# Kernel tuning notes

Hardware: AMD Instinct MI355X
Metric: run time of the kernel (lower is better)

The kernel has to match this reference:

```python
import jax, jax.numpy as jnp
import numpy as np

B, C, N, K, OUT = 8, 64, 40962, 7, 64

def setup_inputs() -> dict:
    key = jax.random.key(0)
    k1, k2, k3, k4 = jax.random.split(key, 4)
    x = jax.random.normal(k1, (B, C, N), dtype=jnp.float32)
    neigh_orders = jax.random.randint(k2, (K * N,), 0, N, dtype=jnp.int64)
    # nn.Linear(7*C, OUT): W [OUT, 7*C], b [OUT]
    W = jax.random.normal(k3, (OUT, K * C), dtype=jnp.float32) * (1.0 / np.sqrt(K * C))
    b = jax.random.normal(k4, (OUT,), dtype=jnp.float32) * 0.01
    return {"x": x, "neigh_orders": neigh_orders, "W": W, "b": b}

def reference(x, neigh_orders, W, b):
    Bn, Cn, Nn = x.shape
    # gather 7-ring neighborhood: [B, C, N*7] -> [B, C, N, 7]
    mat = x[:, :, neigh_orders].reshape(Bn, Cn, Nn, K)
    # torch flattens (7, C) with 7 outer after permute -> W reshaped to [OUT, 7, C]
    W3 = W.reshape(W.shape[0], K, Cn)
    # fused gather-GEMM: [B,C,N,7] x [O,7,C] -> [B,O,N]
    out = jnp.einsum('bcnk,okc->bon', mat, W3) + b[None, :, None]
    return out
```

## Files before the change

kernel.cpp:

```cpp
#include <hip/hip_runtime.h>
#include <hip/hip_bf16.h>

#define Bn   8
#define Cn   64
#define Nn   40962
#define Kn   7
#define OUTn 64
#define NVT  641

typedef __bf16 bf16x8 __attribute__((ext_vector_type(8)));
typedef __bf16 bf16x4 __attribute__((ext_vector_type(4)));
typedef float  f32x4  __attribute__((ext_vector_type(4)));

__global__ __launch_bounds__(256) void transpose_kernel(
    const float* __restrict__ x, __bf16* __restrict__ xT,
    const float* __restrict__ W, __bf16* __restrict__ Wb, int b0)
{
    __shared__ unsigned int tile[64][65];
    const int tid  = threadIdx.x;
    const int lane = tid & 63;
    const int w    = tid >> 6;
    const int n0   = blockIdx.x * 128;
    const int bl   = blockIdx.y;
    const int b    = b0 + bl;
    const size_t xb = (size_t)b * Cn * Nn;

    if (bl == 0) {
        const int wi = blockIdx.x * 256 + tid;
        if (wi < OUTn * Kn * Cn) Wb[wi] = (__bf16)W[wi];
    }

    const int n = n0 + lane * 2;
    if (n < Nn) {
#pragma unroll
        for (int i = 0; i < 16; ++i) {
            const int c = w * 16 + i;
            const float2 v = *(const float2*)(x + xb + (size_t)c * Nn + n);
            const unsigned short ua =
                __builtin_bit_cast(unsigned short, (__bf16)v.x);
            const unsigned short ub =
                __builtin_bit_cast(unsigned short, (__bf16)v.y);
            tile[c][lane] = ((unsigned)ub << 16) | (unsigned)ua;
        }
    }
    __syncthreads();

    const int rsub = lane >> 3;
    const int cblk = lane & 7;
#pragma unroll
    for (int it = 0; it < 4; ++it) {
        const int row = it * 32 + w * 8 + rsub;
        const int n1  = n0 + row;
        if (n1 < Nn) {
            const int slot = row >> 1;
            const int sh   = (row & 1) * 16;
            bf16x8 frag;
#pragma unroll
            for (int e = 0; e < 8; ++e) {
                const unsigned u = tile[cblk * 8 + e][slot];
                frag[e] = __builtin_bit_cast(
                    __bf16, (unsigned short)((u >> sh) & 0xffffu));
            }
            *(bf16x8*)(xT + ((size_t)bl * Nn + n1) * Cn + cblk * 8) = frag;
        }
    }
}

__global__ __launch_bounds__(256, 2) void gconv_kernel(
    const __bf16* __restrict__ xT,
    const int*    __restrict__ nbr,
    const __bf16* __restrict__ Wb,
    const float*  __restrict__ bias,
    float*        __restrict__ out)
{
    __shared__ __bf16 sbuf[Kn][64][64];

    const int blk  = blockIdx.x;
    const int bl   = blk & 7;
    const int grp  = blk >> 3;
    const int w    = threadIdx.x >> 6;
    const int l    = threadIdx.x & 63;
    const int col  = l & 15;
    const int quad = l >> 4;
    const int rme  = l >> 3;
    const int srcoff = ((l & 7) ^ rme) * 16;
    const int wv   = w & 1;
    const int wo   = w >> 1;
    const __bf16* xb = xT + (size_t)bl * Nn * Cn;

    bf16x8 aW[2][14];
#pragma unroll
    for (int s = 0; s < 2; ++s)
#pragma unroll
        for (int kc = 0; kc < 14; ++kc)
            aW[s][kc] = *(const bf16x8*)(Wb
                + (size_t)((wo * 2 + s) * 16 + col) * (Kn * Cn)
                + kc * 32 + quad * 8);

    float bv[2][4];
#pragma unroll
    for (int s = 0; s < 2; ++s)
#pragma unroll
        for (int r4 = 0; r4 < 4; ++r4)
            bv[s][r4] = bias[(wo * 2 + s) * 16 + quad * 4 + r4];

#define LOADIDX(vt_, dst_)                                                    \
    {                                                                         \
        _Pragma("unroll")                                                     \
        for (int j = 0; j < 2; ++j) {                                         \
            int v = (vt_)*64 + w * 16 + j * 8 + rme;                          \
            if (v > Nn - 1) v = Nn - 1;                                       \
            _Pragma("unroll")                                                 \
            for (int kn = 0; kn < Kn; ++kn) {                                 \
                int id = nbr[v * 7 + kn];                                     \
                id = id < 0 ? 0 : (id >= Nn ? Nn - 1 : id);                   \
                dst_[j][kn] = id * (Cn * 2);                                  \
            }                                                                 \
        }                                                                     \
    }

    int ofsA[2][Kn];
    LOADIDX(grp, ofsA)

    for (int vt = grp; vt < NVT; vt += 64) {
        __syncthreads();

#pragma unroll
        for (int kn = 0; kn < Kn; ++kn) {
#pragma unroll
            for (int j = 0; j < 2; ++j) {
                const char* src_ = (const char*)xb + ofsA[j][kn] + srcoff;
                __builtin_amdgcn_global_load_lds(
                    (const unsigned int*)src_,
                    (unsigned int*)&sbuf[kn][w * 16 + j * 8][0], 16, 0, 0);
            }
        }

        int ofsB[2][Kn];
        LOADIDX(vt + 64, ofsB)

        __syncthreads();

        f32x4 acc[2][2];
#pragma unroll
        for (int s = 0; s < 2; ++s)
#pragma unroll
            for (int t = 0; t < 2; ++t)
                acc[s][t] = (f32x4){0.f, 0.f, 0.f, 0.f};

        __builtin_amdgcn_s_setprio(1);
#pragma unroll
        for (int kn = 0; kn < Kn; ++kn) {
#pragma unroll
            for (int h = 0; h < 2; ++h) {
                const int q = h * 4 + quad;
#pragma unroll
                for (int t = 0; t < 2; ++t) {
                    const int r    = (wv * 2 + t) * 16 + col;
                    const int slot = q ^ (r & 7);
                    const bf16x8 bf = *(const bf16x8*)&sbuf[kn][r][slot * 8];
#pragma unroll
                    for (int s = 0; s < 2; ++s)
                        acc[s][t] = __builtin_amdgcn_mfma_f32_16x16x32_bf16(
                            aW[s][kn * 2 + h], bf, acc[s][t], 0, 0, 0);
                }
            }
        }
        __builtin_amdgcn_s_setprio(0);

        const int v0 = vt * 64;
#pragma unroll
        for (int s = 0; s < 2; ++s) {
#pragma unroll
            for (int r4 = 0; r4 < 4; ++r4) {
                const int o = (wo * 2 + s) * 16 + quad * 4 + r4;
#pragma unroll
                for (int t = 0; t < 2; ++t) {
                    const int n = v0 + (wv * 2 + t) * 16 + col;
                    if (n < Nn)
                        out[((size_t)bl * OUTn + o) * Nn + n] =
                            acc[s][t][r4] + bv[s][r4];
                }
            }
        }

#pragma unroll
        for (int j = 0; j < 2; ++j)
#pragma unroll
            for (int kn = 0; kn < Kn; ++kn)
                ofsA[j][kn] = ofsB[j][kn];
    }
#undef LOADIDX
}

__global__ __launch_bounds__(256) void naive_kernel(
    const float* __restrict__ x, const int* __restrict__ nbr,
    const float* __restrict__ W, const float* __restrict__ bias,
    float* __restrict__ out)
{
    __shared__ float xs[4][Kn * Cn];
    const int v = threadIdx.x >> 6;
    const int o = threadIdx.x & 63;
    const int b = blockIdx.y;
    const int n = blockIdx.x * 4 + v;
    const bool ok = n < Nn;
    const int nn = ok ? n : 0;

#pragma unroll
    for (int k = 0; k < Kn; ++k) {
        int id = nbr[nn * Kn + k];
        id = id < 0 ? 0 : (id >= Nn ? Nn - 1 : id);
        xs[v][k * Cn + o] = x[((size_t)b * Cn + o) * Nn + id];
    }
    __syncthreads();

    float acc = bias[o];
    for (int j = 0; j < Kn * Cn; ++j)
        acc += W[o * (Kn * Cn) + j] * xs[v][j];

    if (ok)
        out[((size_t)b * OUTn + o) * Nn + n] = acc;
}

extern "C" void kernel_launch(void* const* d_in, const int* in_sizes, int n_in,
                              void* d_out, int out_size, void* d_ws, size_t ws_size,
                              hipStream_t stream)
{
    const float* x    = (const float*)d_in[0];
    const int*   nbr  = (const int*)d_in[1];
    const float* W    = (const float*)d_in[2];
    const float* bias = (const float*)d_in[3];
    float*       out  = (float*)d_out;

    const size_t w_bytes     = (size_t)OUTn * Kn * Cn * sizeof(__bf16);
    const size_t batch_bytes = (size_t)Nn * Cn * sizeof(__bf16);
    int nb = 0;
    if (ws_size > w_bytes)
        nb = (int)((ws_size - w_bytes) / batch_bytes);
    if (nb > Bn) nb = Bn;

    if (nb >= Bn) {
        __bf16* Wb = (__bf16*)d_ws;
        __bf16* xT = (__bf16*)((char*)d_ws + w_bytes);

        dim3 tgrid((Nn + 127) / 128, Bn);
        transpose_kernel<<<tgrid, 256, 0, stream>>>(x, xT, W, Wb, 0);
        gconv_kernel<<<512, 256, 0, stream>>>(xT, nbr, Wb, bias, out);
    } else {
        dim3 ngrid((Nn + 3) / 4, Bn);
        naive_kernel<<<ngrid, 256, 0, stream>>>(x, nbr, W, bias, out);
    }
}
```

Before: 202.2 us.

## Double-buffer gathered LDS tiles with 32-vertex tiles and more blocks

The gather-GEMM kernel now stages 32-vertex tiles into a double-buffered LDS array. The next tile's async global-to-LDS gather is issued before computing the current one, with a partial vmcnt wait and raw barriers. Tile size is halved and the grid doubled to 1024 blocks, so the load latency of the random-neighbour gathers overlaps MFMA work. In exchange there are fewer MFMAs per barrier and more index loads per output, and correctness rests on the hand-written waitcnt count.

```diff
diff --git a/kernel.cpp b/kernel.cpp
--- a/kernel.cpp
+++ b/kernel.cpp
@@ -6,7 +6,8 @@
 #define Nn   40962
 #define Kn   7
 #define OUTn 64
-#define NVT  641
+#define NVT32  1281
+#define GROUPS 128
 
 typedef __bf16 bf16x8 __attribute__((ext_vector_type(8)));
 typedef __bf16 bf16x4 __attribute__((ext_vector_type(4)));
@@ -73,7 +74,7 @@
     const float*  __restrict__ bias,
     float*        __restrict__ out)
 {
-    __shared__ __bf16 sbuf[Kn][64][64];
+    __shared__ __bf16 sbuf[2][Kn][32][64];
 
     const int blk  = blockIdx.x;
     const int bl   = blk & 7;
@@ -106,91 +107,82 @@
 
 #define LOADIDX(vt_, dst_)                                                    \
     {                                                                         \
+        int v = (vt_)*32 + w * 8 + rme;                                       \
+        if (v > Nn - 1) v = Nn - 1;                                           \
         _Pragma("unroll")                                                     \
-        for (int j = 0; j < 2; ++j) {                                         \
-            int v = (vt_)*64 + w * 16 + j * 8 + rme;                          \
-            if (v > Nn - 1) v = Nn - 1;                                       \
-            _Pragma("unroll")                                                 \
-            for (int kn = 0; kn < Kn; ++kn) {                                 \
-                int id = nbr[v * 7 + kn];                                     \
-                id = id < 0 ? 0 : (id >= Nn ? Nn - 1 : id);                   \
-                dst_[j][kn] = id * (Cn * 2);                                  \
-            }                                                                 \
+        for (int kn = 0; kn < Kn; ++kn) {                                     \
+            int id = nbr[v * 7 + kn];                                         \
+            id = id < 0 ? 0 : (id >= Nn ? Nn - 1 : id);                       \
+            dst_[kn] = id * (Cn * 2);                                         \
         }                                                                     \
     }
 
-    int ofsA[2][Kn];
-    LOADIDX(grp, ofsA)
-
-    for (int vt = grp; vt < NVT; vt += 64) {
-        __syncthreads();
-
+#define STAGE(p_, ofs_)                                                       \
+    {                                                                         \
+        _Pragma("unroll")                                                     \
+        for (int kn = 0; kn < Kn; ++kn) {                                     \
+            const char* src_ = (const char*)xb + ofs_[kn] + srcoff;           \
+            __builtin_amdgcn_global_load_lds(                                 \
+                (const unsigned int*)src_,                                    \
+                (unsigned int*)&sbuf[p_][kn][w * 8][0], 16, 0, 0);            \
+        }                                                                     \
+    }
+
+    int ofsC[Kn];
+    LOADIDX(grp, ofsC)
+    __builtin_amdgcn_sched_barrier(0);
+    STAGE(0, ofsC)
+    __builtin_amdgcn_sched_barrier(0);
+    LOADIDX(grp + GROUPS, ofsC)
+
+    int p = 0;
+    for (int vt = grp; vt < NVT32; vt += GROUPS) {
+        __builtin_amdgcn_s_barrier();
+        __builtin_amdgcn_sched_barrier(0);
+        STAGE(p ^ 1, ofsC)
+        __builtin_amdgcn_sched_barrier(0);
+        asm volatile("s_waitcnt vmcnt(7)" ::: "memory");
+        __builtin_amdgcn_s_barrier();
+        __builtin_amdgcn_sched_barrier(0);
+
+        LOADIDX(vt + 2 * GROUPS, ofsC)
+
+        f32x4 acc[2];
+        acc[0] = (f32x4){0.f, 0.f, 0.f, 0.f};
+        acc[1] = (f32x4){0.f, 0.f, 0.f, 0.f};
+
+        __builtin_amdgcn_s_setprio(1);
 #pragma unroll
         for (int kn = 0; kn < Kn; ++kn) {
 #pragma unroll
-            for (int j = 0; j < 2; ++j) {
-                const char* src_ = (const char*)xb + ofsA[j][kn] + srcoff;
-                __builtin_amdgcn_global_load_lds(
-                    (const unsigned int*)src_,
-                    (unsigned int*)&sbuf[kn][w * 16 + j * 8][0], 16, 0, 0);
+            for (int h = 0; h < 2; ++h) {
+                const int q    = h * 4 + quad;
+                const int slot = q ^ (col & 7);
+                const bf16x8 bf =
+                    *(const bf16x8*)&sbuf[p][kn][wv * 16 + col][slot * 8];
+#pragma unroll
+                for (int s = 0; s < 2; ++s)
+                    acc[s] = __builtin_amdgcn_mfma_f32_16x16x32_bf16(
+                        aW[s][kn * 2 + h], bf, acc[s], 0, 0, 0);
             }
         }
-
-        int ofsB[2][Kn];
-        LOADIDX(vt + 64, ofsB)
-
-        __syncthreads();
-
-        f32x4 acc[2][2];
-#pragma unroll
-        for (int s = 0; s < 2; ++s)
-#pragma unroll
-            for (int t = 0; t < 2; ++t)
-                acc[s][t] = (f32x4){0.f, 0.f, 0.f, 0.f};
-
-        __builtin_amdgcn_s_setprio(1);
-#pragma unroll
-        for (int kn = 0; kn < Kn; ++kn) {
-#pragma unroll
-            for (int h = 0; h < 2; ++h) {
-                const int q = h * 4 + quad;
-#pragma unroll
-                for (int t = 0; t < 2; ++t) {
-                    const int r    = (wv * 2 + t) * 16 + col;
-                    const int slot = q ^ (r & 7);
-                    const bf16x8 bf = *(const bf16x8*)&sbuf[kn][r][slot * 8];
-#pragma unroll
-                    for (int s = 0; s < 2; ++s)
-                        acc[s][t] = __builtin_amdgcn_mfma_f32_16x16x32_bf16(
-                            aW[s][kn * 2 + h], bf, acc[s][t], 0, 0, 0);
+        __builtin_amdgcn_s_setprio(0);
+
+        const int n = vt * 32 + wv * 16 + col;
+        if (n < Nn) {
+#pragma unroll
+            for (int s = 0; s < 2; ++s)
+#pragma unroll
+                for (int r4 = 0; r4 < 4; ++r4) {
+                    const int o = (wo * 2 + s) * 16 + quad * 4 + r4;
+                    out[((size_t)bl * OUTn + o) * Nn + n] =
+                        acc[s][r4] + bv[s][r4];
                 }
-            }
-        }
-        __builtin_amdgcn_s_setprio(0);
-
-        const int v0 = vt * 64;
-#pragma unroll
-        for (int s = 0; s < 2; ++s) {
-#pragma unroll
-            for (int r4 = 0; r4 < 4; ++r4) {
-                const int o = (wo * 2 + s) * 16 + quad * 4 + r4;
-#pragma unroll
-                for (int t = 0; t < 2; ++t) {
-                    const int n = v0 + (wv * 2 + t) * 16 + col;
-                    if (n < Nn)
-                        out[((size_t)bl * OUTn + o) * Nn + n] =
-                            acc[s][t][r4] + bv[s][r4];
-                }
-            }
-        }
-
-#pragma unroll
-        for (int j = 0; j < 2; ++j)
-#pragma unroll
-            for (int kn = 0; kn < Kn; ++kn)
-                ofsA[j][kn] = ofsB[j][kn];
+        }
+        p ^= 1;
     }
 #undef LOADIDX
+#undef STAGE
 }
 
 __global__ __launch_bounds__(256) void naive_kernel(
@@ -245,7 +237,7 @@
 
         dim3 tgrid((Nn + 127) / 128, Bn);
         transpose_kernel<<<tgrid, 256, 0, stream>>>(x, xT, W, Wb, 0);
-        gconv_kernel<<<512, 256, 0, stream>>>(xT, nbr, Wb, bias, out);
+        gconv_kernel<<<Bn * GROUPS, 256, 0, stream>>>(xT, nbr, Wb, bias, out);
     } else {
         dim3 ngrid((Nn + 3) / 4, Bn);
         naive_kernel<<<ngrid, 256, 0, stream>>>(x, nbr, W, bias, out);
```

After: 215.7 us. +6.7%, slower.
